# Performance work log

Measured on AMD Instinct MI355X. Metric: run time of the kernel, lower is better.

The kernel has to match this reference:

```python
import jax, jax.numpy as jnp
import numpy as np

G, KS = 8, 3          # groups, kernel size
K = KS * KS           # sampling points per group
OM = 32               # per-group offset_mask dim: ceil(3K/8)*8
EPS = 1e-5


def setup_inputs() -> dict:
    key = jax.random.key(0)
    ks = jax.random.split(key, 12)
    N, C, H, W = 4, 128, 64, 64
    x = jax.random.normal(ks[0], (N, C, H, W), jnp.float32)
    w_value = jax.random.normal(ks[1], (C, C), jnp.float32) / np.sqrt(C)
    b_value = jax.random.normal(ks[2], (C,), jnp.float32) * 0.01
    # small offset weights -> modest sampling offsets (real module inits these to 0)
    w_off = jax.random.normal(ks[3], (C, G * OM), jnp.float32) * 0.02
    b_off = jax.random.normal(ks[4], (G * OM,), jnp.float32) * 0.01
    w_out = jax.random.normal(ks[5], (C, C), jnp.float32) / np.sqrt(C)
    b_out = jax.random.normal(ks[6], (C,), jnp.float32) * 0.01
    bn_gamma = jax.random.uniform(ks[7], (C,), jnp.float32, 0.5, 1.5)
    bn_beta = jax.random.normal(ks[8], (C,), jnp.float32) * 0.1
    bn_mean = jax.random.normal(ks[9], (C,), jnp.float32) * 0.1
    bn_var = jax.random.uniform(ks[10], (C,), jnp.float32, 0.5, 1.5)
    return dict(x=x, w_value=w_value, b_value=b_value, w_off=w_off, b_off=b_off,
                w_out=w_out, b_out=b_out, bn_gamma=bn_gamma, bn_beta=bn_beta,
                bn_mean=bn_mean, bn_var=bn_var)


def _dcnv4(x, w_value, b_value, w_off, b_off, w_out, b_out,
           bn_gamma, bn_beta, bn_mean, bn_var):
    N, C, H, W = x.shape
    Cg = C // G
    P = H * W
    xf = x.transpose(0, 2, 3, 1).reshape(N, P, C)              # N,P,C (channels-last tokens)
    val = xf @ w_value + b_value                               # value projection
    om = (xf @ w_off + b_off).reshape(N, P, G, OM)             # offsets+mask (padded to 32)
    offset = om[..., :2 * K].reshape(N, P, G, K, 2)            # (dx, dy) pairs
    mask = om[..., 2 * K:3 * K]                                # modulation, NO softmax (DCNv4)

    # base sampling grid: output pixel + centered 3x3 footprint (stride 1, dil 1)
    py, px = jnp.meshgrid(jnp.arange(H), jnp.arange(W), indexing='ij')
    kk = jnp.arange(KS) - (KS - 1) // 2
    ky, kx = jnp.meshgrid(kk, kk, indexing='ij')
    base_y = (py.reshape(-1)[:, None] + ky.reshape(-1)[None, :]).astype(x.dtype)  # P,K
    base_x = (px.reshape(-1)[:, None] + kx.reshape(-1)[None, :]).astype(x.dtype)
    sy = base_y[None, :, None, :] + offset[..., 1]             # N,P,G,K sampling y
    sx = base_x[None, :, None, :] + offset[..., 0]             # N,P,G,K sampling x

    vflat = val.reshape(N, P, G, Cg).transpose(0, 2, 1, 3)     # N,G,P,Cg

    def gather(iy, ix):
        lin = jnp.clip(iy, 0, H - 1) * W + jnp.clip(ix, 0, W - 1)   # N,P,G,K
        lin = lin.transpose(0, 2, 1, 3).reshape(N, G, P * K)
        g = jnp.take_along_axis(vflat, lin[..., None], axis=2)      # N,G,P*K,Cg
        return g.reshape(N, G, P, K, Cg).transpose(0, 2, 1, 3, 4)   # N,P,G,K,Cg

    y0 = jnp.floor(sy); x0 = jnp.floor(sx)
    ty = sy - y0; tx = sx - x0
    y0i = y0.astype(jnp.int32); x0i = x0.astype(jnp.int32)

    def valid(iy, ix):
        return ((iy >= 0) & (iy < H) & (ix >= 0) & (ix < W)).astype(x.dtype)

    acc = jnp.zeros((N, P, G, K, Cg), x.dtype)
    for dy, dx, wgt in ((0, 0, (1 - ty) * (1 - tx)), (0, 1, (1 - ty) * tx),
                        (1, 0, ty * (1 - tx)), (1, 1, ty * tx)):
        iy, ix = y0i + dy, x0i + dx
        acc = acc + gather(iy, ix) * (wgt * valid(iy, ix))[..., None]

    out = (acc * mask[..., None]).sum(axis=3)                  # aggregate over K -> N,P,G,Cg
    out = out.reshape(N, P, C) @ w_out + b_out                 # output projection
    out = out.reshape(N, H, W, C).transpose(0, 3, 1, 2)        # back to NCHW

    # BatchNorm (inference) + SiLU
    inv = bn_gamma / jnp.sqrt(bn_var + EPS)
    out = out * inv[None, :, None, None] + (bn_beta - bn_mean * inv)[None, :, None, None]
    return out * jax.nn.sigmoid(out)


def reference(x, w_value, b_value, w_off, b_off, w_out, b_out,
              bn_gamma, bn_beta, bn_mean, bn_var):
    return _dcnv4(x, w_value, b_value, w_off, b_off, w_out, b_out,
                  bn_gamma, bn_beta, bn_mean, bn_var)
```

## Files before the change

### kernel.cpp

```cpp
#include <hip/hip_runtime.h>
#include <cstdint>

typedef __bf16 v8bf __attribute__((ext_vector_type(8)));
typedef float f32x4 __attribute__((ext_vector_type(4)));

#define BN_EPS 1e-5f

__device__ __forceinline__ float b2f(uint32_t u) {
    union { uint32_t i; float f; } v; v.i = u << 16; return v.f;
}
__device__ __forceinline__ uint16_t f2b(float f) {
    uint32_t u = __builtin_bit_cast(uint32_t, f);
    u += 0x7fffu + ((u >> 16) & 1u);
    return (uint16_t)(u >> 16);
}

__global__ void prep_kernel(const float* __restrict__ wv, const float* __restrict__ wo,
                            const float* __restrict__ wout,
                            const float* __restrict__ gamma, const float* __restrict__ beta,
                            const float* __restrict__ mean, const float* __restrict__ var,
                            uint16_t* __restrict__ wT, float* __restrict__ bnc) {
    int idx = blockIdx.x * 256 + threadIdx.x;
    if (idx < 512 * 128) {
        int r = idx >> 7, ci = idx & 127;
        float v;
        if (r < 128)      v = wv[ci * 128 + r];
        else if (r < 384) v = wo[ci * 256 + (r - 128)];
        else              v = wout[ci * 128 + (r - 384)];
        wT[idx] = f2b(v);
    }
    if (idx < 128) {
        float inv = gamma[idx] * rsqrtf(var[idx] + BN_EPS);
        bnc[idx] = inv;
        bnc[128 + idx] = beta[idx] - mean[idx] * inv;
    }
}

__global__ void transpose_kernel(const float* __restrict__ x, uint16_t* __restrict__ xf) {
    __shared__ float lds[64 * 65];
    int bid = blockIdx.x;
    int cb = bid & 1, pb = (bid >> 1) & 63, n = bid >> 7;
    int c0 = cb * 64, p0 = pb * 64;
    int l = threadIdx.x & 63, q = threadIdx.x >> 6;
    const float* xp = x + ((size_t)(n * 128 + c0)) * 4096 + p0;
#pragma unroll
    for (int i = 0; i < 16; i++) {
        int c = i * 4 + q;
        lds[l * 65 + c] = xp[(size_t)c * 4096 + l];
    }
    __syncthreads();
#pragma unroll
    for (int i = 0; i < 16; i++) {
        int pr = i * 4 + q;
        xf[((size_t)(n * 4096 + p0 + pr)) * 128 + c0 + l] = f2b(lds[pr * 65 + l]);
    }
}

__launch_bounds__(256)
__global__ void gemm1_kernel(const uint16_t* __restrict__ xf, const uint16_t* __restrict__ wT,
                             const float* __restrict__ b_value, const float* __restrict__ b_off,
                             uint16_t* __restrict__ valb, uint16_t* __restrict__ omb) {
    __shared__ __align__(16) uint16_t ldsX[128 * 136];
    __shared__ __align__(16) uint16_t ldsW[64 * 136];
    int ct = blockIdx.x;
    int pt = blockIdx.y;
    int p0 = pt * 128, cbase = ct * 64;
    int tid = threadIdx.x;
    int col16 = tid & 15, rowq = tid >> 4;

    const uint4* xg = (const uint4*)xf;
    uint4* lx = (uint4*)ldsX;
#pragma unroll
    for (int i = 0; i < 8; i++) {
        int row = i * 16 + rowq;
        lx[row * 17 + col16] = xg[(size_t)(p0 + row) * 16 + col16];
    }
    const uint4* wg = (const uint4*)wT;
    uint4* lw = (uint4*)ldsW;
#pragma unroll
    for (int i = 0; i < 4; i++) {
        int row = i * 16 + rowq;
        lw[row * 17 + col16] = wg[(size_t)(cbase + row) * 16 + col16];
    }
    __syncthreads();

    int wv = tid >> 6, lane = tid & 63;
    int ln = lane & 15, quad = lane >> 4;
    int cW = cbase + wv * 16 + quad * 4;
    f32x4 binit;
    if (cW < 128) binit = f32x4{b_value[cW], b_value[cW + 1], b_value[cW + 2], b_value[cW + 3]};
    else          binit = f32x4{b_off[cW - 128], b_off[cW - 127], b_off[cW - 126], b_off[cW - 125]};
    f32x4 acc[8];
#pragma unroll
    for (int t = 0; t < 8; t++) acc[t] = binit;

#pragma unroll
    for (int kk = 0; kk < 4; kk++) {
        v8bf a = *(const v8bf*)&ldsW[(wv * 16 + ln) * 136 + kk * 32 + quad * 8];
#pragma unroll
        for (int t = 0; t < 8; t++) {
            v8bf b = *(const v8bf*)&ldsX[(t * 16 + ln) * 136 + kk * 32 + quad * 8];
            acc[t] = __builtin_amdgcn_mfma_f32_16x16x32_bf16(a, b, acc[t], 0, 0, 0);
        }
    }

    int nimg = p0 >> 12, pin0 = p0 & 4095;
    if (cW < 128) {
        int g = cW >> 4, cg = cW & 15;
#pragma unroll
        for (int t = 0; t < 8; t++) {
            int p = pin0 + t * 16 + ln;
            uint32_t u0 = (uint32_t)f2b(acc[t][0]) | ((uint32_t)f2b(acc[t][1]) << 16);
            uint32_t u1 = (uint32_t)f2b(acc[t][2]) | ((uint32_t)f2b(acc[t][3]) << 16);
            *(uint2*)&valb[(((size_t)(nimg * 8 + g) * 4096 + p) << 4) + cg] = make_uint2(u0, u1);
        }
    } else {
        int j0 = cW - 128;
#pragma unroll
        for (int t = 0; t < 8; t++) {
            int p = pin0 + t * 16 + ln;
            uint32_t u0 = (uint32_t)f2b(acc[t][0]) | ((uint32_t)f2b(acc[t][1]) << 16);
            uint32_t u1 = (uint32_t)f2b(acc[t][2]) | ((uint32_t)f2b(acc[t][3]) << 16);
            *(uint2*)&omb[((size_t)(nimg * 4096 + p) << 8) + j0] = make_uint2(u0, u1);
        }
    }
}

__launch_bounds__(256)
__global__ void gather_kernel(const uint16_t* __restrict__ omb, const uint16_t* __restrict__ valb,
                              uint16_t* __restrict__ accb) {
    int tid = threadIdx.x, bid = blockIdx.x;
    int n = bid >> 7, pch = bid & 127;
    int g = tid & 7, pl = tid >> 3;
    int p = pch * 32 + pl;
    int py = p >> 6, px = p & 63;

    const uint16_t* op = omb + (((size_t)(n * 4096 + p)) << 8) + g * 32;
    uint4 q0 = *(const uint4*)(op);
    uint4 q1 = *(const uint4*)(op + 8);
    uint4 q2 = *(const uint4*)(op + 16);
    uint2 q3 = *(const uint2*)(op + 24);
    uint32_t w[14] = {q0.x, q0.y, q0.z, q0.w, q1.x, q1.y, q1.z, q1.w,
                      q2.x, q2.y, q2.z, q2.w, q3.x, q3.y};
    float o[28];
#pragma unroll
    for (int i = 0; i < 14; i++) { o[2 * i] = b2f(w[i] & 0xffff); o[2 * i + 1] = b2f(w[i] >> 16); }

    float acc[16];
#pragma unroll
    for (int i = 0; i < 16; i++) acc[i] = 0.f;

    const uint4* vb = (const uint4*)(valb + ((size_t)(n * 8 + g) << 16));
#pragma unroll
    for (int k = 0; k < 9; k++) {
        float sx = (float)(px + (k % 3) - 1) + o[2 * k];
        float sy = (float)(py + (k / 3) - 1) + o[2 * k + 1];
        float m = o[18 + k];
        float x0f = floorf(sx), y0f = floorf(sy);
        float tx = sx - x0f, ty = sy - y0f;
        int x0 = (int)x0f, y0 = (int)y0f;
#pragma unroll
        for (int dy = 0; dy < 2; dy++) {
            int iy = y0 + dy;
            if (iy < 0 || iy > 63) continue;
            float wy = dy ? ty : 1.f - ty;
#pragma unroll
            for (int dx = 0; dx < 2; dx++) {
                int ix = x0 + dx;
                if (ix < 0 || ix > 63) continue;
                float wgt = m * wy * (dx ? tx : 1.f - tx);
                const uint4* vp = vb + ((size_t)(iy * 64 + ix)) * 2;
                uint4 v0 = vp[0], v1 = vp[1];
                acc[0]  += wgt * b2f(v0.x & 0xffff); acc[1]  += wgt * b2f(v0.x >> 16);
                acc[2]  += wgt * b2f(v0.y & 0xffff); acc[3]  += wgt * b2f(v0.y >> 16);
                acc[4]  += wgt * b2f(v0.z & 0xffff); acc[5]  += wgt * b2f(v0.z >> 16);
                acc[6]  += wgt * b2f(v0.w & 0xffff); acc[7]  += wgt * b2f(v0.w >> 16);
                acc[8]  += wgt * b2f(v1.x & 0xffff); acc[9]  += wgt * b2f(v1.x >> 16);
                acc[10] += wgt * b2f(v1.y & 0xffff); acc[11] += wgt * b2f(v1.y >> 16);
                acc[12] += wgt * b2f(v1.z & 0xffff); acc[13] += wgt * b2f(v1.z >> 16);
                acc[14] += wgt * b2f(v1.w & 0xffff); acc[15] += wgt * b2f(v1.w >> 16);
            }
        }
    }
    uint32_t u[8];
#pragma unroll
    for (int i = 0; i < 8; i++)
        u[i] = (uint32_t)f2b(acc[2 * i]) | ((uint32_t)f2b(acc[2 * i + 1]) << 16);
    uint4* outp = (uint4*)(accb + ((size_t)(n * 4096 + p)) * 128 + g * 16);
    outp[0] = make_uint4(u[0], u[1], u[2], u[3]);
    outp[1] = make_uint4(u[4], u[5], u[6], u[7]);
}

__launch_bounds__(256)
__global__ void gemm3_kernel(const uint16_t* __restrict__ accb, const uint16_t* __restrict__ wT,
                             const float* __restrict__ b_out, const float* __restrict__ bnc,
                             float* __restrict__ out) {
    __shared__ __align__(16) uint16_t ldsA[128 * 136];
    __shared__ __align__(16) uint16_t ldsW[64 * 136];
    int ct = blockIdx.x;
    int pt = blockIdx.y;
    int p0 = pt * 128, cbase = ct * 64;
    int tid = threadIdx.x;
    int col16 = tid & 15, rowq = tid >> 4;

    const uint4* ag = (const uint4*)accb;
    uint4* la = (uint4*)ldsA;
#pragma unroll
    for (int i = 0; i < 8; i++) {
        int row = i * 16 + rowq;
        la[row * 17 + col16] = ag[(size_t)(p0 + row) * 16 + col16];
    }
    const uint4* wg = (const uint4*)wT;
    uint4* lw = (uint4*)ldsW;
#pragma unroll
    for (int i = 0; i < 4; i++) {
        int row = i * 16 + rowq;
        lw[row * 17 + col16] = wg[(size_t)(384 + cbase + row) * 16 + col16];
    }
    __syncthreads();

    int wv = tid >> 6, lane = tid & 63;
    int ln = lane & 15, quad = lane >> 4;
    f32x4 acc[2][4];
#pragma unroll
    for (int ni = 0; ni < 4; ni++) {
        float b = b_out[cbase + ni * 16 + ln];
        acc[0][ni] = f32x4{b, b, b, b};
        acc[1][ni] = f32x4{b, b, b, b};
    }
#pragma unroll
    for (int kk = 0; kk < 4; kk++) {
        v8bf a0 = *(const v8bf*)&ldsA[((wv * 2 + 0) * 16 + ln) * 136 + kk * 32 + quad * 8];
        v8bf a1 = *(const v8bf*)&ldsA[((wv * 2 + 1) * 16 + ln) * 136 + kk * 32 + quad * 8];
#pragma unroll
        for (int ni = 0; ni < 4; ni++) {
            v8bf b = *(const v8bf*)&ldsW[(ni * 16 + ln) * 136 + kk * 32 + quad * 8];
            acc[0][ni] = __builtin_amdgcn_mfma_f32_16x16x32_bf16(a0, b, acc[0][ni], 0, 0, 0);
            acc[1][ni] = __builtin_amdgcn_mfma_f32_16x16x32_bf16(a1, b, acc[1][ni], 0, 0, 0);
        }
    }
    int nimg = p0 >> 12, pin0 = p0 & 4095;
#pragma unroll
    for (int mi = 0; mi < 2; mi++) {
        int p = pin0 + (wv * 2 + mi) * 16 + quad * 4;
#pragma unroll
        for (int ni = 0; ni < 4; ni++) {
            int cc = cbase + ni * 16 + ln;
            float inv = bnc[cc], add = bnc[128 + cc];
            float4 r;
            float* rp = &r.x;
#pragma unroll
            for (int q = 0; q < 4; q++) {
                float z = acc[mi][ni][q] * inv + add;
                rp[q] = z / (1.f + __expf(-z));
            }
            *(float4*)&out[((size_t)(nimg * 128 + cc) << 12) + p] = r;
        }
    }
}

extern "C" void kernel_launch(void* const* d_in, const int* in_sizes, int n_in,
                              void* d_out, int out_size, void* d_ws, size_t ws_size,
                              hipStream_t stream) {
    const float* x       = (const float*)d_in[0];
    const float* w_value = (const float*)d_in[1];
    const float* b_value = (const float*)d_in[2];
    const float* w_off   = (const float*)d_in[3];
    const float* b_off   = (const float*)d_in[4];
    const float* w_out   = (const float*)d_in[5];
    const float* b_out   = (const float*)d_in[6];
    const float* gamma   = (const float*)d_in[7];
    const float* beta    = (const float*)d_in[8];
    const float* mean    = (const float*)d_in[9];
    const float* var     = (const float*)d_in[10];
    float* out = (float*)d_out;

    char* ws = (char*)d_ws;
    uint16_t* xf   = (uint16_t*)(ws);
    uint16_t* accb = (uint16_t*)(ws + ((size_t)4 << 20));
    uint16_t* valb = (uint16_t*)(ws + ((size_t)8 << 20));
    uint16_t* omb  = (uint16_t*)(ws + ((size_t)12 << 20));
    uint16_t* wT   = (uint16_t*)(ws + ((size_t)20 << 20));
    float*    bnc  = (float*)(ws + ((size_t)20 << 20) + (1 << 18));

    hipLaunchKernelGGL(prep_kernel, dim3(256), dim3(256), 0, stream,
                       w_value, w_off, w_out, gamma, beta, mean, var, wT, bnc);
    hipLaunchKernelGGL(transpose_kernel, dim3(512), dim3(256), 0, stream, x, xf);
    hipLaunchKernelGGL(gemm1_kernel, dim3(6, 128), dim3(256), 0, stream,
                       xf, wT, b_value, b_off, valb, omb);
    hipLaunchKernelGGL(gather_kernel, dim3(512), dim3(256), 0, stream, omb, valb, accb);
    hipLaunchKernelGGL(gemm3_kernel, dim3(2, 128), dim3(256), 0, stream,
                       accb, wT, b_out, bnc, out);
}
```

Baseline: 115.3 us.

## Fuse gather into output GEMM via LDS and merge prep with transpose

The bilinear gather now writes its bf16 aggregated tile straight into LDS, and the same block then runs the output-projection MFMA GEMM plus BN+SiLU epilogue. This removes the accb global round trip and one launch. Weight prep is folded into the transpose kernel as extra blocks, saving another launch. In exchange the gather runs on only 256 blocks, each doing two pixel rows per thread. That lowers parallelism and occupancy for the latency-bound gather, and each block reloads the full output weight into LDS.

Result: slower. 118.6 us (+2.8%).

```diff
diff --git a/kernel.cpp b/kernel.cpp
--- a/kernel.cpp
+++ b/kernel.cpp
@@ -15,44 +15,46 @@
     return (uint16_t)(u >> 16);
 }
 
-__global__ void prep_kernel(const float* __restrict__ wv, const float* __restrict__ wo,
-                            const float* __restrict__ wout,
-                            const float* __restrict__ gamma, const float* __restrict__ beta,
-                            const float* __restrict__ mean, const float* __restrict__ var,
-                            uint16_t* __restrict__ wT, float* __restrict__ bnc) {
-    int idx = blockIdx.x * 256 + threadIdx.x;
-    if (idx < 512 * 128) {
-        int r = idx >> 7, ci = idx & 127;
-        float v;
-        if (r < 128)      v = wv[ci * 128 + r];
-        else if (r < 384) v = wo[ci * 256 + (r - 128)];
-        else              v = wout[ci * 128 + (r - 384)];
-        wT[idx] = f2b(v);
-    }
-    if (idx < 128) {
-        float inv = gamma[idx] * rsqrtf(var[idx] + BN_EPS);
-        bnc[idx] = inv;
-        bnc[128 + idx] = beta[idx] - mean[idx] * inv;
-    }
-}
-
-__global__ void transpose_kernel(const float* __restrict__ x, uint16_t* __restrict__ xf) {
-    __shared__ float lds[64 * 65];
+__global__ void prep_transpose_kernel(const float* __restrict__ x,
+                                      const float* __restrict__ wv, const float* __restrict__ wo,
+                                      const float* __restrict__ wout,
+                                      const float* __restrict__ gamma, const float* __restrict__ beta,
+                                      const float* __restrict__ mean, const float* __restrict__ var,
+                                      uint16_t* __restrict__ xf, uint16_t* __restrict__ wT,
+                                      float* __restrict__ bnc) {
     int bid = blockIdx.x;
-    int cb = bid & 1, pb = (bid >> 1) & 63, n = bid >> 7;
-    int c0 = cb * 64, p0 = pb * 64;
-    int l = threadIdx.x & 63, q = threadIdx.x >> 6;
-    const float* xp = x + ((size_t)(n * 128 + c0)) * 4096 + p0;
-#pragma unroll
-    for (int i = 0; i < 16; i++) {
-        int c = i * 4 + q;
-        lds[l * 65 + c] = xp[(size_t)c * 4096 + l];
-    }
-    __syncthreads();
-#pragma unroll
-    for (int i = 0; i < 16; i++) {
-        int pr = i * 4 + q;
-        xf[((size_t)(n * 4096 + p0 + pr)) * 128 + c0 + l] = f2b(lds[pr * 65 + l]);
+    if (bid < 512) {
+        __shared__ float lds[64 * 65];
+        int cb = bid & 1, pb = (bid >> 1) & 63, n = bid >> 7;
+        int c0 = cb * 64, p0 = pb * 64;
+        int l = threadIdx.x & 63, q = threadIdx.x >> 6;
+        const float* xp = x + ((size_t)(n * 128 + c0)) * 4096 + p0;
+#pragma unroll
+        for (int i = 0; i < 16; i++) {
+            int c = i * 4 + q;
+            lds[l * 65 + c] = xp[(size_t)c * 4096 + l];
+        }
+        __syncthreads();
+#pragma unroll
+        for (int i = 0; i < 16; i++) {
+            int pr = i * 4 + q;
+            xf[((size_t)(n * 4096 + p0 + pr)) * 128 + c0 + l] = f2b(lds[pr * 65 + l]);
+        }
+    } else {
+        int idx = (bid - 512) * 256 + threadIdx.x;
+        if (idx < 512 * 128) {
+            int r = idx >> 7, ci = idx & 127;
+            float v;
+            if (r < 128)      v = wv[ci * 128 + r];
+            else if (r < 384) v = wo[ci * 256 + (r - 128)];
+            else              v = wout[ci * 128 + (r - 384)];
+            wT[idx] = f2b(v);
+        }
+        if (idx < 128) {
+            float inv = gamma[idx] * rsqrtf(var[idx] + BN_EPS);
+            bnc[idx] = inv;
+            bnc[128 + idx] = beta[idx] - mean[idx] * inv;
+        }
     }
 }
 
@@ -127,135 +129,123 @@
 }
 
 __launch_bounds__(256)
-__global__ void gather_kernel(const uint16_t* __restrict__ omb, const uint16_t* __restrict__ valb,
-                              uint16_t* __restrict__ accb) {
-    int tid = threadIdx.x, bid = blockIdx.x;
-    int n = bid >> 7, pch = bid & 127;
-    int g = tid & 7, pl = tid >> 3;
-    int p = pch * 32 + pl;
-    int py = p >> 6, px = p & 63;
-
-    const uint16_t* op = omb + (((size_t)(n * 4096 + p)) << 8) + g * 32;
-    uint4 q0 = *(const uint4*)(op);
-    uint4 q1 = *(const uint4*)(op + 8);
-    uint4 q2 = *(const uint4*)(op + 16);
-    uint2 q3 = *(const uint2*)(op + 24);
-    uint32_t w[14] = {q0.x, q0.y, q0.z, q0.w, q1.x, q1.y, q1.z, q1.w,
-                      q2.x, q2.y, q2.z, q2.w, q3.x, q3.y};
-    float o[28];
-#pragma unroll
-    for (int i = 0; i < 14; i++) { o[2 * i] = b2f(w[i] & 0xffff); o[2 * i + 1] = b2f(w[i] >> 16); }
-
-    float acc[16];
-#pragma unroll
-    for (int i = 0; i < 16; i++) acc[i] = 0.f;
-
+__global__ void gather_gemm3_kernel(const uint16_t* __restrict__ omb, const uint16_t* __restrict__ valb,
+                                    const uint16_t* __restrict__ wT,
+                                    const float* __restrict__ b_out, const float* __restrict__ bnc,
+                                    float* __restrict__ out) {
+    __shared__ __align__(16) uint16_t ldsA[64 * 136];
+    __shared__ __align__(16) uint16_t ldsW[128 * 136];
+    int pt = blockIdx.x;
+    int p0 = pt * 64;
+    int n = p0 >> 12, pin0 = p0 & 4095;
+    int tid = threadIdx.x;
+
+    {
+        int col16 = tid & 15, rowq = tid >> 4;
+        const uint4* wg = (const uint4*)wT;
+        uint4* lw = (uint4*)ldsW;
+#pragma unroll
+        for (int i = 0; i < 8; i++) {
+            int row = i * 16 + rowq;
+            lw[row * 17 + col16] = wg[(size_t)(384 + row) * 16 + col16];
+        }
+    }
+
+    int g = tid >> 5, pl = tid & 31;
     const uint4* vb = (const uint4*)(valb + ((size_t)(n * 8 + g) << 16));
 #pragma unroll
-    for (int k = 0; k < 9; k++) {
-        float sx = (float)(px + (k % 3) - 1) + o[2 * k];
-        float sy = (float)(py + (k / 3) - 1) + o[2 * k + 1];
-        float m = o[18 + k];
-        float x0f = floorf(sx), y0f = floorf(sy);
-        float tx = sx - x0f, ty = sy - y0f;
-        int x0 = (int)x0f, y0 = (int)y0f;
-#pragma unroll
-        for (int dy = 0; dy < 2; dy++) {
-            int iy = y0 + dy;
-            if (iy < 0 || iy > 63) continue;
-            float wy = dy ? ty : 1.f - ty;
-#pragma unroll
-            for (int dx = 0; dx < 2; dx++) {
-                int ix = x0 + dx;
-                if (ix < 0 || ix > 63) continue;
-                float wgt = m * wy * (dx ? tx : 1.f - tx);
-                const uint4* vp = vb + ((size_t)(iy * 64 + ix)) * 2;
-                uint4 v0 = vp[0], v1 = vp[1];
-                acc[0]  += wgt * b2f(v0.x & 0xffff); acc[1]  += wgt * b2f(v0.x >> 16);
-                acc[2]  += wgt * b2f(v0.y & 0xffff); acc[3]  += wgt * b2f(v0.y >> 16);
-                acc[4]  += wgt * b2f(v0.z & 0xffff); acc[5]  += wgt * b2f(v0.z >> 16);
-                acc[6]  += wgt * b2f(v0.w & 0xffff); acc[7]  += wgt * b2f(v0.w >> 16);
-                acc[8]  += wgt * b2f(v1.x & 0xffff); acc[9]  += wgt * b2f(v1.x >> 16);
-                acc[10] += wgt * b2f(v1.y & 0xffff); acc[11] += wgt * b2f(v1.y >> 16);
-                acc[12] += wgt * b2f(v1.z & 0xffff); acc[13] += wgt * b2f(v1.z >> 16);
-                acc[14] += wgt * b2f(v1.w & 0xffff); acc[15] += wgt * b2f(v1.w >> 16);
+    for (int pp = 0; pp < 2; pp++) {
+        int prow = pp * 32 + pl;
+        int p = p0 + prow;
+        int pin = p & 4095;
+        int py = pin >> 6, px = pin & 63;
+
+        const uint16_t* op = omb + ((size_t)p << 8) + g * 32;
+        uint4 q0 = *(const uint4*)(op);
+        uint4 q1 = *(const uint4*)(op + 8);
+        uint4 q2 = *(const uint4*)(op + 16);
+        uint2 q3 = *(const uint2*)(op + 24);
+        uint32_t w[14] = {q0.x, q0.y, q0.z, q0.w, q1.x, q1.y, q1.z, q1.w,
+                          q2.x, q2.y, q2.z, q2.w, q3.x, q3.y};
+        float o[28];
+#pragma unroll
+        for (int i = 0; i < 14; i++) { o[2 * i] = b2f(w[i] & 0xffff); o[2 * i + 1] = b2f(w[i] >> 16); }
+
+        float acc[16];
+#pragma unroll
+        for (int i = 0; i < 16; i++) acc[i] = 0.f;
+
+#pragma unroll
+        for (int k = 0; k < 9; k++) {
+            float sx = (float)(px + (k % 3) - 1) + o[2 * k];
+            float sy = (float)(py + (k / 3) - 1) + o[2 * k + 1];
+            float m = o[18 + k];
+            float x0f = floorf(sx), y0f = floorf(sy);
+            float tx = sx - x0f, ty = sy - y0f;
+            int x0 = (int)x0f, y0 = (int)y0f;
+#pragma unroll
+            for (int dy = 0; dy < 2; dy++) {
+                int iy = y0 + dy;
+                if (iy < 0 || iy > 63) continue;
+                float wy = dy ? ty : 1.f - ty;
+#pragma unroll
+                for (int dx = 0; dx < 2; dx++) {
+                    int ix = x0 + dx;
+                    if (ix < 0 || ix > 63) continue;
+                    float wgt = m * wy * (dx ? tx : 1.f - tx);
+                    const uint4* vp = vb + ((size_t)(iy * 64 + ix)) * 2;
+                    uint4 v0 = vp[0], v1 = vp[1];
+                    acc[0]  += wgt * b2f(v0.x & 0xffff); acc[1]  += wgt * b2f(v0.x >> 16);
+                    acc[2]  += wgt * b2f(v0.y & 0xffff); acc[3]  += wgt * b2f(v0.y >> 16);
+                    acc[4]  += wgt * b2f(v0.z & 0xffff); acc[5]  += wgt * b2f(v0.z >> 16);
+                    acc[6]  += wgt * b2f(v0.w & 0xffff); acc[7]  += wgt * b2f(v0.w >> 16);
+                    acc[8]  += wgt * b2f(v1.x & 0xffff); acc[9]  += wgt * b2f(v1.x >> 16);
+                    acc[10] += wgt * b2f(v1.y & 0xffff); acc[11] += wgt * b2f(v1.y >> 16);
+                    acc[12] += wgt * b2f(v1.z & 0xffff); acc[13] += wgt * b2f(v1.z >> 16);
+                    acc[14] += wgt * b2f(v1.w & 0xffff); acc[15] += wgt * b2f(v1.w >> 16);
+                }
             }
         }
-    }
-    uint32_t u[8];
-#pragma unroll
-    for (int i = 0; i < 8; i++)
-        u[i] = (uint32_t)f2b(acc[2 * i]) | ((uint32_t)f2b(acc[2 * i + 1]) << 16);
-    uint4* outp = (uint4*)(accb + ((size_t)(n * 4096 + p)) * 128 + g * 16);
-    outp[0] = make_uint4(u[0], u[1], u[2], u[3]);
-    outp[1] = make_uint4(u[4], u[5], u[6], u[7]);
-}
-
-__launch_bounds__(256)
-__global__ void gemm3_kernel(const uint16_t* __restrict__ accb, const uint16_t* __restrict__ wT,
-                             const float* __restrict__ b_out, const float* __restrict__ bnc,
-                             float* __restrict__ out) {
-    __shared__ __align__(16) uint16_t ldsA[128 * 136];
-    __shared__ __align__(16) uint16_t ldsW[64 * 136];
-    int ct = blockIdx.x;
-    int pt = blockIdx.y;
-    int p0 = pt * 128, cbase = ct * 64;
-    int tid = threadIdx.x;
-    int col16 = tid & 15, rowq = tid >> 4;
-
-    const uint4* ag = (const uint4*)accb;
-    uint4* la = (uint4*)ldsA;
-#pragma unroll
-    for (int i = 0; i < 8; i++) {
-        int row = i * 16 + rowq;
-        la[row * 17 + col16] = ag[(size_t)(p0 + row) * 16 + col16];
-    }
-    const uint4* wg = (const uint4*)wT;
-    uint4* lw = (uint4*)ldsW;
-#pragma unroll
-    for (int i = 0; i < 4; i++) {
-        int row = i * 16 + rowq;
-        lw[row * 17 + col16] = wg[(size_t)(384 + cbase + row) * 16 + col16];
+        uint32_t u[8];
+#pragma unroll
+        for (int i = 0; i < 8; i++)
+            u[i] = (uint32_t)f2b(acc[2 * i]) | ((uint32_t)f2b(acc[2 * i + 1]) << 16);
+        uint4* outp = (uint4*)&ldsA[prow * 136 + g * 16];
+        outp[0] = make_uint4(u[0], u[1], u[2], u[3]);
+        outp[1] = make_uint4(u[4], u[5], u[6], u[7]);
     }
     __syncthreads();
 
     int wv = tid >> 6, lane = tid & 63;
     int ln = lane & 15, quad = lane >> 4;
-    f32x4 acc[2][4];
-#pragma unroll
-    for (int ni = 0; ni < 4; ni++) {
-        float b = b_out[cbase + ni * 16 + ln];
-        acc[0][ni] = f32x4{b, b, b, b};
-        acc[1][ni] = f32x4{b, b, b, b};
+    f32x4 acc[8];
+#pragma unroll
+    for (int ni = 0; ni < 8; ni++) {
+        float b = b_out[ni * 16 + ln];
+        acc[ni] = f32x4{b, b, b, b};
     }
 #pragma unroll
     for (int kk = 0; kk < 4; kk++) {
-        v8bf a0 = *(const v8bf*)&ldsA[((wv * 2 + 0) * 16 + ln) * 136 + kk * 32 + quad * 8];
-        v8bf a1 = *(const v8bf*)&ldsA[((wv * 2 + 1) * 16 + ln) * 136 + kk * 32 + quad * 8];
-#pragma unroll
-        for (int ni = 0; ni < 4; ni++) {
+        v8bf a = *(const v8bf*)&ldsA[(wv * 16 + ln) * 136 + kk * 32 + quad * 8];
+#pragma unroll
+        for (int ni = 0; ni < 8; ni++) {
             v8bf b = *(const v8bf*)&ldsW[(ni * 16 + ln) * 136 + kk * 32 + quad * 8];
-            acc[0][ni] = __builtin_amdgcn_mfma_f32_16x16x32_bf16(a0, b, acc[0][ni], 0, 0, 0);
-            acc[1][ni] = __builtin_amdgcn_mfma_f32_16x16x32_bf16(a1, b, acc[1][ni], 0, 0, 0);
-        }
-    }
-    int nimg = p0 >> 12, pin0 = p0 & 4095;
-#pragma unroll
-    for (int mi = 0; mi < 2; mi++) {
-        int p = pin0 + (wv * 2 + mi) * 16 + quad * 4;
-#pragma unroll
-        for (int ni = 0; ni < 4; ni++) {
-            int cc = cbase + ni * 16 + ln;
-            float inv = bnc[cc], add = bnc[128 + cc];
-            float4 r;
-            float* rp = &r.x;
-#pragma unroll
-            for (int q = 0; q < 4; q++) {
-                float z = acc[mi][ni][q] * inv + add;
-                rp[q] = z / (1.f + __expf(-z));
-            }
-            *(float4*)&out[((size_t)(nimg * 128 + cc) << 12) + p] = r;
-        }
+            acc[ni] = __builtin_amdgcn_mfma_f32_16x16x32_bf16(a, b, acc[ni], 0, 0, 0);
+        }
+    }
+    int p = pin0 + wv * 16 + quad * 4;
+#pragma unroll
+    for (int ni = 0; ni < 8; ni++) {
+        int cc = ni * 16 + ln;
+        float inv = bnc[cc], add = bnc[128 + cc];
+        float4 r;
+        float* rp = &r.x;
+#pragma unroll
+        for (int q = 0; q < 4; q++) {
+            float z = acc[ni][q] * inv + add;
+            rp[q] = z / (1.f + __expf(-z));
+        }
+        *(float4*)&out[((size_t)(n * 128 + cc) << 12) + p] = r;
     }
 }
 
@@ -277,18 +267,15 @@
 
     char* ws = (char*)d_ws;
     uint16_t* xf   = (uint16_t*)(ws);
-    uint16_t* accb = (uint16_t*)(ws + ((size_t)4 << 20));
     uint16_t* valb = (uint16_t*)(ws + ((size_t)8 << 20));
     uint16_t* omb  = (uint16_t*)(ws + ((size_t)12 << 20));
     uint16_t* wT   = (uint16_t*)(ws + ((size_t)20 << 20));
     float*    bnc  = (float*)(ws + ((size_t)20 << 20) + (1 << 18));
 
-    hipLaunchKernelGGL(prep_kernel, dim3(256), dim3(256), 0, stream,
-                       w_value, w_off, w_out, gamma, beta, mean, var, wT, bnc);
-    hipLaunchKernelGGL(transpose_kernel, dim3(512), dim3(256), 0, stream, x, xf);
+    hipLaunchKernelGGL(prep_transpose_kernel, dim3(768), dim3(256), 0, stream,
+                       x, w_value, w_off, w_out, gamma, beta, mean, var, xf, wT, bnc);
     hipLaunchKernelGGL(gemm1_kernel, dim3(6, 128), dim3(256), 0, stream,
                        xf, wT, b_value, b_off, valb, omb);
-    hipLaunchKernelGGL(gather_kernel, dim3(512), dim3(256), 0, stream, omb, valb, accb);
-    hipLaunchKernelGGL(gemm3_kernel, dim3(2, 128), dim3(256), 0, stream,
-                       accb, wT, b_out, bnc, out);
-}
+    hipLaunchKernelGGL(gather_gemm3_kernel, dim3(256), dim3(256), 0, stream,
+                       omb, valb, wT, b_out, bnc, out);
+}
```
